# Optimization experiments

Measured on AMD Instinct MI355X. Metric: run time of the kernel, lower is better.

## Reference

```python
import jax, jax.numpy as jnp
import numpy as np

T_STEPS = 16
B, C, H, W = 16, 128, 32, 32
NUM_THRESHOLDS = 8


def setup_inputs() -> dict:
    key = jax.random.key(0)
    x = jax.random.normal(key, ((T_STEPS + 1) * B, C, H, W), dtype=jnp.float32)
    thresh = jnp.array(1.0, dtype=jnp.float32)
    return {"x": x, "thresh": thresh, "T": T_STEPS}


def reference(x, thresh, T):
    K = NUM_THRESHOLDS
    Bt = x.shape[0] // (T + 1)
    xt = x.reshape((T + 1, Bt) + x.shape[1:])  # [T+1, B, C, H, W]

    # thre_shaped[k] = thresh / 2**k ; threshold for firing = 0.75 * thre_shaped
    thre_vec = thresh / (2.0 ** jnp.arange(K, dtype=x.dtype))  # [K]
    thre_shaped = thre_vec.reshape((K,) + (1,) * xt[0].ndim)    # [K,1,1,1,1]
    thre_threshold = thre_shaped * 0.75

    bias = xt[0]

    def step(carry, inp):
        mem, exp_in, exp_out = carry
        xi, t = inp  # t = 1..T (float)
        mem = mem + xi - bias + exp_in - exp_out
        pos = (mem[None] >= thre_threshold).astype(x.dtype)   # [K,B,C,H,W]
        neg = (mem[None] <= -thre_threshold).astype(x.dtype)
        # pos_true[0]=pos[0]; pos_true[k]=pos[k]-pos[k-1]  (first-fired threshold)
        pos_true = jnp.concatenate([pos[:1], pos[1:] - pos[:-1]], axis=0)
        neg_true = jnp.concatenate([neg[:1], neg[1:] - neg[:-1]], axis=0)
        spike = jnp.sum(thre_shaped * (pos_true - neg_true), axis=0)
        mem = mem - spike
        exp_in = exp_in + (xi - bias) / t
        exp_out = exp_out + spike / t
        return (mem, exp_in, exp_out), spike

    init = (jnp.zeros_like(bias), bias, jnp.zeros_like(bias))
    ts = jnp.arange(1, T + 1, dtype=x.dtype)
    _, spikes = jax.lax.scan(step, init, (xt[1:], ts))

    out = jnp.concatenate([jnp.zeros_like(xt[:1]), spikes], axis=0)
    return out.reshape(x.shape)
```

## Files before the change

### kernel.cpp

```cpp
#include <hip/hip_runtime.h>


#define T_STEPS 16
#define K_THRESH 8

typedef float v2f __attribute__((ext_vector_type(2)));

__global__ __launch_bounds__(256, 8) void snn_scan_kernel(
    const float* __restrict__ x,
    const float* __restrict__ thresh_p,
    float* __restrict__ out,
    int N2)
{
    const int i = blockIdx.x * blockDim.x + threadIdx.x;
    if (i >= N2) return;

    const float th = *thresh_p;
    const float thq0 = 0.75f * th;
    float thq[K_THRESH];
#pragma unroll
    for (int k = 0; k < K_THRESH; ++k) thq[k] = __builtin_ldexpf(thq0, -k);

    const v2f* __restrict__ xv = (const v2f*)x;
    v2f* __restrict__ ov = (v2f*)out;

    const v2f b2 = xv[i];
    {
        v2f z; z.x = 0.f; z.y = 0.f;
        __builtin_nontemporal_store(z, ov + i);
    }

    float mem0 = 0.f, mem1 = 0.f;
    const float bias0 = b2.x, bias1 = b2.y;
    float ein0 = bias0, ein1 = bias1;
    float eout0 = 0.f, eout1 = 0.f;

    v2f xi2 = xv[N2 + i];

#pragma unroll
    for (int t = 1; t <= T_STEPS; ++t) {
        const float xi0 = xi2.x, xi1 = xi2.y;
        if (t < T_STEPS) xi2 = xv[(t + 1) * N2 + i];

        const bool tp2 = (t & (t - 1)) == 0;
        const float rt = 1.0f / (float)t;
        const float q_t = tp2 ? (th * rt)
                              : (th / (float)t);

        auto stepj = [&](float& mem, float& ein, float& eout,
                         float xi, float bias) -> float {
            const float m = (((mem + xi) - bias) + ein) - eout;
            const float a = __builtin_fabsf(m);
            float sc = 0.f;
#pragma unroll
            for (int k = K_THRESH - 1; k >= 0; --k) {
                const float sck = (float)(1.0 / (double)(1 << k));
                sc = (a >= thq[k]) ? sck : sc;
            }
            const bool pos = (m >= 0.f);
            const float mag = sc * th;
            const float s   = pos ? mag : -mag;
            const float sq  = sc * q_t;
            mem = m - s;
            const float d = xi - bias;
            if (tp2) ein = ein + d * rt;
            else     ein = ein + d / (float)t;
            eout = eout + (pos ? sq : -sq);
            return s;
        };

        v2f sp;
        sp.x = stepj(mem0, ein0, eout0, xi0, bias0);
        sp.y = stepj(mem1, ein1, eout1, xi1, bias1);
        __builtin_nontemporal_store(sp, ov + t * N2 + i);
    }
}

extern "C" void kernel_launch(void* const* d_in, const int* in_sizes, int n_in,
                              void* d_out, int out_size, void* d_ws, size_t ws_size,
                              hipStream_t stream) {
    const float* x      = (const float*)d_in[0];
    const float* thresh = (const float*)d_in[1];
    float* out = (float*)d_out;

    const int N  = in_sizes[0] / (T_STEPS + 1);
    const int N2 = N / 2;

    const int block = 256;
    const int grid  = (N2 + block - 1) / block;
    snn_scan_kernel<<<grid, block, 0, stream>>>(x, thresh, out, N2);
}
```

Baseline: 251.4 us.

## Compute threshold level via exponent bit arithmetic and preload all timesteps

Replaces the 8-way compare/select chain over thresholds with integer arithmetic on the float bit pattern: the threshold index comes from the exponent difference, and the spike magnitude is built by subtracting from the exponent bits. It also loads all 16 timestep inputs into registers up front and precomputes the th/t reciprocals for odd divisors. This cuts ALU work per element and exposes all loads at once, at the cost of higher register use. The bit trick assumes normal floats and power-of-two threshold ratios.

```diff
diff --git a/kernel.cpp b/kernel.cpp
--- a/kernel.cpp
+++ b/kernel.cpp
@@ -2,7 +2,6 @@
 
 
 #define T_STEPS 16
-#define K_THRESH 8
 
 typedef float v2f __attribute__((ext_vector_type(2)));
 
@@ -15,16 +14,22 @@
     const int i = blockIdx.x * blockDim.x + threadIdx.x;
     if (i >= N2) return;
 
-    const float th = *thresh_p;
-    const float thq0 = 0.75f * th;
-    float thq[K_THRESH];
-#pragma unroll
-    for (int k = 0; k < K_THRESH; ++k) thq[k] = __builtin_ldexpf(thq0, -k);
-
     const v2f* __restrict__ xv = (const v2f*)x;
     v2f* __restrict__ ov = (v2f*)out;
 
     const v2f b2 = xv[i];
+    v2f buf[T_STEPS];
+#pragma unroll
+    for (int t = 0; t < T_STEPS; ++t) buf[t] = xv[(t + 1) * N2 + i];
+
+    const float th = *thresh_p;
+    const unsigned vbits  = __float_as_uint(0.75f * th);
+    const unsigned thbits = __float_as_uint(th);
+
+    const float q3 = th / 3.0f,  q5 = th / 5.0f,  q7 = th / 7.0f,
+                q9 = th / 9.0f,  q11 = th / 11.0f, q13 = th / 13.0f,
+                q15 = th / 15.0f;
+
     {
         v2f z; z.x = 0.f; z.y = 0.f;
         __builtin_nontemporal_store(z, ov + i);
@@ -35,37 +40,48 @@
     float ein0 = bias0, ein1 = bias1;
     float eout0 = 0.f, eout1 = 0.f;
 
-    v2f xi2 = xv[N2 + i];
-
 #pragma unroll
     for (int t = 1; t <= T_STEPS; ++t) {
-        const float xi0 = xi2.x, xi1 = xi2.y;
-        if (t < T_STEPS) xi2 = xv[(t + 1) * N2 + i];
+        const float xi0 = buf[t - 1].x, xi1 = buf[t - 1].y;
 
-        const bool tp2 = (t & (t - 1)) == 0;
-        const float rt = 1.0f / (float)t;
-        const float q_t = tp2 ? (th * rt)
-                              : (th / (float)t);
+        const bool  tp2 = (t & (t - 1)) == 0;
+        const float rt  = 1.0f / (float)t;
+        float q_t;
+        switch (t) {
+            case 1: case 2: case 4: case 8: case 16: q_t = th * rt; break;
+            case 3:  q_t = q3;          break;
+            case 5:  q_t = q5;          break;
+            case 6:  q_t = q3 * 0.5f;   break;
+            case 7:  q_t = q7;          break;
+            case 9:  q_t = q9;          break;
+            case 10: q_t = q5 * 0.5f;   break;
+            case 11: q_t = q11;         break;
+            case 12: q_t = q3 * 0.25f;  break;
+            case 13: q_t = q13;         break;
+            case 14: q_t = q7 * 0.5f;   break;
+            default: q_t = q15;         break;
+        }
+        const unsigned qbits = __float_as_uint(q_t);
 
         auto stepj = [&](float& mem, float& ein, float& eout,
                          float xi, float bias) -> float {
             const float m = (((mem + xi) - bias) + ein) - eout;
-            const float a = __builtin_fabsf(m);
-            float sc = 0.f;
-#pragma unroll
-            for (int k = K_THRESH - 1; k >= 0; --k) {
-                const float sck = (float)(1.0 / (double)(1 << k));
-                sc = (a >= thq[k]) ? sck : sc;
-            }
-            const bool pos = (m >= 0.f);
-            const float mag = sc * th;
-            const float s   = pos ? mag : -mag;
-            const float sq  = sc * q_t;
+            const unsigned mb  = __float_as_uint(m);
+            const unsigned u   = mb & 0x7fffffffu;
+            const int diff     = (int)(vbits - u);
+            int k = (diff + 0x7fffff) >> 23;
+            k = k < 0 ? 0 : k;
+            const bool fire = (k <= 7);
+            const unsigned ksh = (unsigned)k << 23;
+            const unsigned sgn = mb & 0x80000000u;
+            const unsigned sb  = fire ? (sgn | (thbits - ksh)) : 0u;
+            const unsigned qb  = fire ? (sgn | (qbits - ksh)) : 0u;
+            const float s = __uint_as_float(sb);
             mem = m - s;
             const float d = xi - bias;
             if (tp2) ein = ein + d * rt;
             else     ein = ein + d / (float)t;
-            eout = eout + (pos ? sq : -sq);
+            eout = eout + __uint_as_float(qb);
             return s;
         };
 
```

Measured after the change: 268.4 us. 6.8% more time.
